# Kernel optimization log

Measured on AMD Instinct MI355X. Metric: run time of the kernel, lower is better.

## Reference

```python
import jax, jax.numpy as jnp
import numpy as np

N_NODES, N_GRAPHS, NODES_PER = 20000, 20, 1000
N_EDGES, N_REL, N_BASES = 320000, 8, 4
FEAT, HID, EMB = 128, 256, 128


def rgcn_conv(x, src, dst, etype, comp, basis, root_w, bias, num_rel, num_nodes):
    # W_r = sum_b comp[r,b] * basis[b]  (basis decomposition)
    W = jnp.einsum('rb,bio->rio', comp, basis)           # [R, in, out]
    xr = jnp.einsum('ni,rio->nro', x, W)                 # [N, R, out]
    msg = xr[src, etype]                                 # [E, out] gather per edge
    # mean aggregation per (dst, relation), as in PyG RGCNConv (aggr='mean')
    key = dst * num_rel + etype
    cnt = jax.ops.segment_sum(jnp.ones(src.shape[0], x.dtype), key,
                              num_segments=num_nodes * num_rel)
    norm = 1.0 / jnp.maximum(cnt, 1.0)
    agg = jax.ops.segment_sum(msg * norm[key][:, None], dst, num_segments=num_nodes)
    return agg + x @ root_w + bias


def setup_inputs() -> dict:
    key = jax.random.key(0)
    ks = jax.random.split(key, 16)
    x = jax.random.normal(ks[0], (N_GRAPHS, HID), jnp.float32)
    edge_attr = jax.random.uniform(ks[1], (N_EDGES, 2), jnp.float32)
    node_x = jax.random.normal(ks[2], (N_NODES, FEAT), jnp.float32)
    edge_index = jax.random.randint(ks[3], (2, N_EDGES), 0, N_NODES)
    edge_type = jax.random.randint(ks[4], (N_EDGES,), 0, N_REL)
    batch = jnp.repeat(jnp.arange(N_GRAPHS), NODES_PER)   # equal-size graphs
    nest_id = jax.random.randint(ks[5], (N_GRAPHS,), 0, N_NODES)
    s1 = 1.0 / np.sqrt(FEAT)
    s2 = 1.0 / np.sqrt(HID)
    comp1 = jax.random.normal(ks[6], (N_REL, N_BASES), jnp.float32) * 0.5
    basis1 = jax.random.normal(ks[7], (N_BASES, FEAT, HID), jnp.float32) * s1
    root1 = jax.random.normal(ks[8], (FEAT, HID), jnp.float32) * s1
    bias1 = jnp.zeros((HID,), jnp.float32)
    comp2 = jax.random.normal(ks[9], (N_REL, N_BASES), jnp.float32) * 0.5
    basis2 = jax.random.normal(ks[10], (N_BASES, HID, EMB), jnp.float32) * s2
    root2 = jax.random.normal(ks[11], (HID, EMB), jnp.float32) * s2
    bias2 = jnp.zeros((EMB,), jnp.float32)
    msg_w = jax.random.normal(ks[12], (HID, EMB), jnp.float32) * s2
    msg_b = jnp.zeros((EMB,), jnp.float32)
    return dict(x=x, edge_attr=edge_attr, node_x=node_x, edge_index=edge_index,
                edge_type=edge_type, batch=batch, nest_id=nest_id,
                comp1=comp1, basis1=basis1, root1=root1, bias1=bias1,
                comp2=comp2, basis2=basis2, root2=root2, bias2=bias2,
                msg_w=msg_w, msg_b=msg_b)


def reference(x, edge_attr, node_x, edge_index, edge_type, batch, nest_id,
              comp1, basis1, root1, bias1, comp2, basis2, root2, bias2,
              msg_w, msg_b):
    N = node_x.shape[0]
    R = comp1.shape[0]
    B = nest_id.shape[0]
    src, dst = edge_index[0], edge_index[1]
    # distance binning (computed in original forward but unused downstream)
    distances = edge_attr[:, 0]
    min_d, max_d = distances.min(), distances.max()
    bin_size = (max_d - min_d) / 3
    _binned = jnp.clip(jnp.floor((distances - min_d) / bin_size), 0, 2)
    # 2-layer RGCN encoder (keep_dims=() -> strip_node_types is identity)
    h = jax.nn.relu(rgcn_conv(node_x, src, dst, edge_type,
                              comp1, basis1, root1, bias1, R, N))
    node_emb = rgcn_conv(h, src, dst, edge_type,
                         comp2, basis2, root2, bias2, R, N)
    nest_emb = node_emb[nest_id]                 # [B, emb]
    rel_node = node_emb - nest_emb[batch]        # [N, emb]
    message_emb = x @ msg_w + msg_b              # [B, emb]
    scores = jnp.sum(rel_node * message_emb[batch], axis=-1)  # [N]
    logits = scores.reshape(B, N // B)
    return jax.nn.log_softmax(logits, axis=-1)
```

## Files before the change

### kernel.cpp

```cpp
#include <hip/hip_runtime.h>
#include <hip/hip_bf16.h>

#define NEDGE 320000
#define NNODE 20000
#define MP    20096
#define NRELS 8
#define FEAT  128
#define HID   256
#define EMB   128
#define NGRAPH 20
#define NPG   1000
#define NBASE 4
#define PAD   96

typedef __attribute__((ext_vector_type(4))) float f32x4;
typedef __attribute__((ext_vector_type(8))) __bf16 bf16x8;
typedef __attribute__((ext_vector_type(8))) unsigned short u16x8;

static __device__ __forceinline__ float bf2f(unsigned short u){
  union { unsigned int i; float f; } v; v.i = ((unsigned int)u) << 16; return v.f;
}
static __device__ __forceinline__ unsigned short f2bf(float f){
  union { float f; unsigned int i; } v; v.f = f;
  unsigned int x = v.i;
  return (unsigned short)((x + 0x7fffu + ((x >> 16) & 1u)) >> 16);
}

__device__ __forceinline__ void load_lds16(const void* g, void* l){
  __builtin_amdgcn_global_load_lds((const __attribute__((address_space(1))) void*)g,
                                   (__attribute__((address_space(3))) void*)l, 16, 0, 0);
}

__global__ void k_zeroMe(int* __restrict__ cursor,
                         const float* __restrict__ x, const float* __restrict__ mw,
                         const float* __restrict__ mb, float* __restrict__ me){
  int blk = blockIdx.x;
  if (blk < 79){
    int i = blk*256 + threadIdx.x;
    if (i < NNODE) cursor[i] = 0;
  } else {
    int id = (blk-79)*256 + threadIdx.x;
    if (id >= NGRAPH*EMB) return;
    int g = id >> 7, e = id & 127;
    float s = mb[e];
    for (int i=0;i<HID;i++) s += x[g*HID + i] * mw[i*EMB + e];
    me[id] = s;
  }
}

__global__ void k_prepScatter(const int* __restrict__ ei, const int* __restrict__ et,
                              int* __restrict__ cursor, unsigned int* __restrict__ spk,
                              const float* __restrict__ xin, unsigned short* __restrict__ xb,
                              const float* __restrict__ basis, const float* __restrict__ root,
                              unsigned short* __restrict__ Bt,
                              const float* __restrict__ basis2, const float* __restrict__ root2,
                              const float* __restrict__ me, float* __restrict__ v){
  int blk = blockIdx.x;
  if (blk < 1250){
    int e = blk*256 + threadIdx.x;
    if (e < NEDGE){
      int src = ei[e];
      int r = et[e];
      int dst = ei[NEDGE + e];
      int pos = atomicAdd(&cursor[dst], 1);
      if (pos < PAD) spk[(size_t)dst*PAD + pos] = (unsigned int)src | ((unsigned int)r << 15);
    }
  } else if (blk < 11250){
    int i = (blk-1250)*256 + threadIdx.x;
    if (i < NNODE*FEAT) xb[i] = f2bf(xin[i]);
  } else if (blk < 11890){
    int idx = (blk-11250)*256 + threadIdx.x;
    if (idx >= 256*640) return;
    int o = idx / 640, k = idx % 640;
    float val = (k < 512) ? basis[(size_t)k*256 + o] : root[(size_t)(k-512)*256 + o];
    Bt[(size_t)o*640 + k] = f2bf(val);
  } else {
    int w = threadIdx.x >> 6, lane = threadIdx.x & 63;
    int id = (blk-11890)*4 + w;
    if (id >= NGRAPH*1280) return;
    int g = id / 1280, k = id % 1280;
    const float* row = (k < 1024) ? (basis2 + (size_t)k*EMB) : (root2 + (size_t)(k-1024)*EMB);
    float2 a = *(const float2*)(row + lane*2);
    float2 m = *(const float2*)(me + g*EMB + lane*2);
    float p = a.x*m.x + a.y*m.y;
    #pragma unroll
    for (int d=32; d; d>>=1) p += __shfl_down(p, d);
    if (lane == 0) v[(size_t)g*1280 + k] = p;
  }
}

__global__ void k_agg1(const unsigned short* __restrict__ xb, const int* __restrict__ cursor,
                       const unsigned int* __restrict__ spk,
                       const float* __restrict__ comp1, unsigned short* __restrict__ s1,
                       const float* __restrict__ v, unsigned short* __restrict__ BtV){
  if (blockIdx.x >= 1250){
    int idx = (blockIdx.x-1250)*256 + threadIdx.x;
    if (idx >= 128*256) return;
    int c = idx >> 8, k = idx & 255;
    float val = 0.f;
    if (c < 80)        val = v[(size_t)(c>>2)*1280 + (c&3)*256 + k];
    else if (c < 100)  val = v[(size_t)(c-80)*1280 + 1024 + k];
    BtV[idx] = f2bf(val);
    return;
  }
  __shared__ float c1s[32];
  __shared__ float wcomb[16*32];
  if (threadIdx.x < 32) c1s[threadIdx.x] = comp1[threadIdx.x];
  __syncthreads();
  int grp = threadIdx.x >> 4, sl = threadIdx.x & 15;
  int n = blockIdx.x*16 + grp;
  int C = cursor[n]; if (C > PAD) C = PAD;
  const unsigned int* pp = spk + (size_t)n*PAD;
  if (sl < 8){
    int c = 0;
    for (int j=0;j<C;j++) c += (int)(((pp[j] >> 15) & 7) == (unsigned)sl);
    float inv = (c > 0) ? __builtin_amdgcn_rcpf((float)c) : 0.f;
    #pragma unroll
    for (int b=0;b<NBASE;b++) wcomb[grp*32 + sl*4 + b] = c1s[sl*4+b]*inv;
  }
  const float* wg = wcomb + grp*32;
  float u[NBASE][8] = {};
  int j = 0;
  for (; j+8 <= C; j += 8){
    unsigned int pk[8];
    u16x8 vv[8];
    #pragma unroll
    for (int t=0;t<8;t++) pk[t] = pp[j+t];
    #pragma unroll
    for (int t=0;t<8;t++) vv[t] = *(const u16x8*)(xb + (size_t)(pk[t] & 0x7FFF)*FEAT + sl*8);
    #pragma unroll
    for (int t=0;t<8;t++){
      const float* cr = wg + ((pk[t] >> 15) & 7)*4;
      #pragma unroll
      for (int b=0;b<NBASE;b++){
        float wb = cr[b];
        #pragma unroll
        for (int k=0;k<8;k++) u[b][k] += wb*bf2f(vv[t][k]);
      }
    }
  }
  for (; j < C; ++j){
    unsigned int pk = pp[j];
    u16x8 vv = *(const u16x8*)(xb + (size_t)(pk & 0x7FFF)*FEAT + sl*8);
    const float* cr = wg + ((pk >> 15) & 7)*4;
    #pragma unroll
    for (int b=0;b<NBASE;b++){
      float wb = cr[b];
      #pragma unroll
      for (int k=0;k<8;k++) u[b][k] += wb*bf2f(vv[k]);
    }
  }
  #pragma unroll
  for (int b=0;b<NBASE;b++){
    u16x8 o8;
    #pragma unroll
    for (int k=0;k<8;k++) o8[k] = f2bf(u[b][k]);
    *(u16x8*)(s1 + (size_t)n*(NBASE*FEAT) + b*FEAT + sl*8) = o8;
  }
}

__global__ __launch_bounds__(256, 4)
void k_gemmHD(const unsigned short* __restrict__ A0,
              const unsigned short* __restrict__ A1,
              const unsigned short* __restrict__ B1t,
              const unsigned short* __restrict__ BtV,
              const float* __restrict__ bias1,
              float* __restrict__ D)
{
  __shared__ __align__(16) unsigned short As[32*64];
  __shared__ __align__(16) unsigned short Bs[128*64];
  __shared__ __align__(16) unsigned short hs[32*256];

  const int tid = threadIdx.x;
  const int w = tid >> 6, lane = tid & 63;
  const int wr = w >> 1, wc = w & 1;
  const int m0 = blockIdx.x * 32;

  for (int half=0; half<2; ++half){
    f32x4 acc[4];
    #pragma unroll
    for (int i=0;i<4;i++) acc[i] = (f32x4){0.f,0.f,0.f,0.f};
    for (int kt=0; kt<10; ++kt){
      const int kb = kt*64;
      {
        const unsigned short* Ab; int ld, kk0;
        if (kb < 512){ Ab = A0; ld = 512; kk0 = kb; } else { Ab = A1; ld = 128; kk0 = kb-512; }
        int row = tid >> 3, slot = tid & 7;
        int srcs = slot ^ (row & 7);
        load_lds16(Ab + (size_t)(m0+row)*ld + kk0 + srcs*8, (char*)As + (w*64)*16);
      }
      #pragma unroll
      for (int t=0;t<4;t++){
        int c = t*256 + tid, row = c >> 3, slot = c & 7;
        int srcs = slot ^ (row & 7);
        load_lds16(B1t + (size_t)(half*128+row)*640 + kb + srcs*8, (char*)Bs + (t*256 + w*64)*16);
      }
      asm volatile("s_waitcnt vmcnt(0)" ::: "memory");
      __syncthreads();
      #pragma unroll
      for (int kk=0;kk<2;++kk){
        int arow = wr*16 + (lane & 15);
        int aslot = (kk*4 + (lane >> 4)) ^ (arow & 7);
        bf16x8 afr = *(const bf16x8*)(As + arow*64 + aslot*8);
        #pragma unroll
        for (int fn=0;fn<4;++fn){
          int brow = wc*64 + fn*16 + (lane & 15);
          int bslot = (kk*4 + (lane >> 4)) ^ (brow & 7);
          bf16x8 bfr = *(const bf16x8*)(Bs + brow*64 + bslot*8);
          acc[fn] = __builtin_amdgcn_mfma_f32_16x16x32_bf16(afr, bfr, acc[fn], 0, 0, 0);
        }
      }
      __syncthreads();
    }
    #pragma unroll
    for (int fn=0;fn<4;++fn){
      int col = half*128 + wc*64 + fn*16 + (lane & 15);
      float b = bias1[col];
      int s = col >> 3;
      #pragma unroll
      for (int q=0;q<4;q++){
        int row = wr*16 + (lane >> 4)*4 + q;
        float val = acc[fn][q] + b;
        val = val > 0.f ? val : 0.f;
        int p = (s & ~7) | ((s & 7) ^ (row & 7));
        hs[row*256 + p*8 + (col & 7)] = f2bf(val);
      }
    }
  }
  __syncthreads();

  f32x4 acc2[4];
  #pragma unroll
  for (int i=0;i<4;i++) acc2[i] = (f32x4){0.f,0.f,0.f,0.f};
  for (int kt=0; kt<4; ++kt){
    const int kb = kt*64;
    #pragma unroll
    for (int t=0;t<4;t++){
      int c = t*256 + tid, row = c >> 3, slot = c & 7;
      int srcs = slot ^ (row & 7);
      load_lds16(BtV + (size_t)row*256 + kb + srcs*8, (char*)Bs + (t*256 + w*64)*16);
    }
    asm volatile("s_waitcnt vmcnt(0)" ::: "memory");
    __syncthreads();
    #pragma unroll
    for (int kk=0;kk<2;++kk){
      int arow = wr*16 + (lane & 15);
      int slog = kt*8 + kk*4 + (lane >> 4);
      int ap = (slog & ~7) | ((slog & 7) ^ (arow & 7));
      bf16x8 afr = *(const bf16x8*)(hs + arow*256 + ap*8);
      #pragma unroll
      for (int fn=0;fn<4;++fn){
        int brow = wc*64 + fn*16 + (lane & 15);
        int bslot = (kk*4 + (lane >> 4)) ^ (brow & 7);
        bf16x8 bfr = *(const bf16x8*)(Bs + brow*64 + bslot*8);
        acc2[fn] = __builtin_amdgcn_mfma_f32_16x16x32_bf16(afr, bfr, acc2[fn], 0, 0, 0);
      }
    }
    __syncthreads();
  }
  #pragma unroll
  for (int fn=0;fn<4;++fn){
    int col = wc*64 + fn*16 + (lane & 15);
    #pragma unroll
    for (int q=0;q<4;q++){
      int row = m0 + wr*16 + (lane >> 4)*4 + q;
      D[(size_t)row*128 + col] = acc2[fn][q];
    }
  }
}

__global__ void k_score2(const float* __restrict__ D, const int* __restrict__ cursor,
                         const unsigned int* __restrict__ spk,
                         const float* __restrict__ comp2, const int* __restrict__ batch,
                         float* __restrict__ sc){
  __shared__ float4 c2s[8];
  __shared__ float4 wc4[16*8];
  if (threadIdx.x < 8) c2s[threadIdx.x] = ((const float4*)comp2)[threadIdx.x];
  __syncthreads();
  int grp = threadIdx.x >> 4, sl = threadIdx.x & 15;
  int n = blockIdx.x*16 + grp;
  if (n >= NNODE) return;
  int g = batch[n];
  int C = cursor[n]; if (C > PAD) C = PAD;
  const unsigned int* pp = spk + (size_t)n*PAD;
  if (sl < 8){
    int c = 0;
    for (int j=0;j<C;j++) c += (int)(((pp[j] >> 15) & 7) == (unsigned)sl);
    float inv = (c > 0) ? __builtin_amdgcn_rcpf((float)c) : 0.f;
    float4 cw = c2s[sl];
    cw.x *= inv; cw.y *= inv; cw.z *= inv; cw.w *= inv;
    wc4[grp*8 + sl] = cw;
  }
  float acc = 0.f;
  for (int j = sl; j < C; j += 16){
    unsigned int pk = pp[j];
    int s = pk & 0x7FFF;
    float4 dv = *(const float4*)(D + (size_t)s*128 + g*4);
    float4 cw = wc4[grp*8 + ((pk >> 15) & 7)];
    acc += cw.x*dv.x + cw.y*dv.y + cw.z*dv.z + cw.w*dv.w;
  }
  #pragma unroll
  for (int d=8; d; d>>=1) acc += __shfl_down(acc, d, 16);
  if (sl == 0) sc[n] = acc + D[(size_t)n*128 + 80 + g];
}

__global__ void k_lsm(const float* __restrict__ sc, float* __restrict__ out){
  __shared__ float sb[1024];
  __shared__ float red[256];
  int g = blockIdx.x, t = threadIdx.x;
  float lm = -1e30f;
  for (int j=t; j<1024; j+=256){
    float v = (j < NPG) ? sc[g*NPG + j] : -1e30f;
    sb[j] = v; lm = fmaxf(lm, v);
  }
  red[t] = lm; __syncthreads();
  for (int off=128; off; off>>=1){ if (t < off) red[t] = fmaxf(red[t], red[t+off]); __syncthreads(); }
  float mx = red[0]; __syncthreads();
  float ls = 0.f;
  for (int j=t; j<1024; j+=256){ if (j < NPG) ls += expf(sb[j] - mx); }
  red[t] = ls; __syncthreads();
  for (int off=128; off; off>>=1){ if (t < off) red[t] += red[t+off]; __syncthreads(); }
  float lse = mx + logf(red[0]);
  for (int j=t; j<NPG; j+=256) out[g*NPG + j] = sb[j] - lse;
}

extern "C" void kernel_launch(void* const* d_in, const int* in_sizes, int n_in,
                              void* d_out, int out_size, void* d_ws, size_t ws_size,
                              hipStream_t stream) {
  const float* x       = (const float*)d_in[0];
  const float* node_x  = (const float*)d_in[2];
  const int*   ei      = (const int*)d_in[3];
  const int*   et      = (const int*)d_in[4];
  const int*   batch   = (const int*)d_in[5];
  const float* comp1   = (const float*)d_in[7];
  const float* basis1  = (const float*)d_in[8];
  const float* root1   = (const float*)d_in[9];
  const float* bias1   = (const float*)d_in[10];
  const float* comp2   = (const float*)d_in[11];
  const float* basis2  = (const float*)d_in[12];
  const float* root2   = (const float*)d_in[13];
  const float* msg_w   = (const float*)d_in[15];
  const float* msg_b   = (const float*)d_in[16];
  float* out = (float*)d_out;

  char* p = (char*)d_ws;
  size_t off = 0;
  auto alloc = [&](size_t bytes) -> char* {
    char* r = p + off;
    off += (bytes + 255) & ~(size_t)255;
    return r;
  };
  int*            cursor = (int*)alloc(NNODE*4);
  unsigned int*   spk    = (unsigned int*)alloc((size_t)NNODE*PAD*4);
  unsigned short* B1t    = (unsigned short*)alloc((size_t)256*640*2);
  unsigned short* BtV    = (unsigned short*)alloc((size_t)128*256*2);
  float*          me     = (float*)alloc(NGRAPH*EMB*4);
  float*          v      = (float*)alloc((size_t)NGRAPH*1280*4);
  unsigned short* xb     = (unsigned short*)alloc((size_t)MP*FEAT*2);
  unsigned short* s1     = (unsigned short*)alloc((size_t)MP*512*2);
  float*          D      = (float*)alloc((size_t)MP*128*4);
  float*          sc     = (float*)alloc(NNODE*4);

  k_zeroMe     <<<89, 256, 0, stream>>>(cursor, x, msg_w, msg_b, me);
  k_prepScatter<<<18290, 256, 0, stream>>>(ei, et, cursor, spk, node_x, xb,
                                           basis1, root1, B1t, basis2, root2, me, v);
  k_agg1  <<<1378, 256, 0, stream>>>(xb, cursor, spk, comp1, s1, v, BtV);
  k_gemmHD<<<628, 256, 0, stream>>>(s1, xb, B1t, BtV, bias1, D);
  k_score2<<<1250, 256, 0, stream>>>(D, cursor, spk, comp2, batch, sc);
  k_lsm   <<<NGRAPH, 256, 0, stream>>>(sc, out);
}
```

Before: 101.4 us.

## Vectorize bf16 conversion and assign one wavefront per node in aggregation

The fp32-to-bf16 conversion of node features now processes four elements per thread with float4 loads and ushort4 stores, so it needs fewer blocks. The layer-1 aggregation kernel now gives each node a full 64-lane wavefront, each lane handling two features, instead of a 16-thread group with eight features per lane. This gives more parallelism, fewer registers per lane and fully coalesced 256-byte row gathers. In exchange, the per-edge index loads and the relation-count loop are repeated per wavefront, there are four times as many blocks, and each gather is narrower (4 bytes per lane).

```diff
diff --git a/kernel.cpp b/kernel.cpp
--- a/kernel.cpp
+++ b/kernel.cpp
@@ -19,6 +19,12 @@
 
 static __device__ __forceinline__ float bf2f(unsigned short u){
   union { unsigned int i; float f; } v; v.i = ((unsigned int)u) << 16; return v.f;
+}
+static __device__ __forceinline__ float bflo(unsigned int u){
+  union { unsigned int i; float f; } v; v.i = u << 16; return v.f;
+}
+static __device__ __forceinline__ float bfhi(unsigned int u){
+  union { unsigned int i; float f; } v; v.i = u & 0xFFFF0000u; return v.f;
 }
 static __device__ __forceinline__ unsigned short f2bf(float f){
   union { float f; unsigned int i; } v; v.f = f;
@@ -65,18 +71,23 @@
       int pos = atomicAdd(&cursor[dst], 1);
       if (pos < PAD) spk[(size_t)dst*PAD + pos] = (unsigned int)src | ((unsigned int)r << 15);
     }
-  } else if (blk < 11250){
-    int i = (blk-1250)*256 + threadIdx.x;
-    if (i < NNODE*FEAT) xb[i] = f2bf(xin[i]);
-  } else if (blk < 11890){
-    int idx = (blk-11250)*256 + threadIdx.x;
+  } else if (blk < 3750){
+    int i = (blk-1250)*1024 + threadIdx.x*4;
+    if (i < NNODE*FEAT){
+      float4 f = *(const float4*)(xin + i);
+      ushort4 o;
+      o.x = f2bf(f.x); o.y = f2bf(f.y); o.z = f2bf(f.z); o.w = f2bf(f.w);
+      *(ushort4*)(xb + i) = o;
+    }
+  } else if (blk < 4390){
+    int idx = (blk-3750)*256 + threadIdx.x;
     if (idx >= 256*640) return;
     int o = idx / 640, k = idx % 640;
     float val = (k < 512) ? basis[(size_t)k*256 + o] : root[(size_t)(k-512)*256 + o];
     Bt[(size_t)o*640 + k] = f2bf(val);
   } else {
     int w = threadIdx.x >> 6, lane = threadIdx.x & 63;
-    int id = (blk-11890)*4 + w;
+    int id = (blk-4390)*4 + w;
     if (id >= NGRAPH*1280) return;
     int g = id / 1280, k = id % 1280;
     const float* row = (k < 1024) ? (basis2 + (size_t)k*EMB) : (root2 + (size_t)(k-1024)*EMB);
@@ -93,8 +104,8 @@
                        const unsigned int* __restrict__ spk,
                        const float* __restrict__ comp1, unsigned short* __restrict__ s1,
                        const float* __restrict__ v, unsigned short* __restrict__ BtV){
-  if (blockIdx.x >= 1250){
-    int idx = (blockIdx.x-1250)*256 + threadIdx.x;
+  if (blockIdx.x >= 5000){
+    int idx = (blockIdx.x-5000)*256 + threadIdx.x;
     if (idx >= 128*256) return;
     int c = idx >> 8, k = idx & 255;
     float val = 0.f;
@@ -104,58 +115,51 @@
     return;
   }
   __shared__ float c1s[32];
-  __shared__ float wcomb[16*32];
+  __shared__ float wcomb[4][32];
   if (threadIdx.x < 32) c1s[threadIdx.x] = comp1[threadIdx.x];
   __syncthreads();
-  int grp = threadIdx.x >> 4, sl = threadIdx.x & 15;
-  int n = blockIdx.x*16 + grp;
+  int w = threadIdx.x >> 6, lane = threadIdx.x & 63;
+  int n = blockIdx.x*4 + w;
   int C = cursor[n]; if (C > PAD) C = PAD;
   const unsigned int* pp = spk + (size_t)n*PAD;
-  if (sl < 8){
+  if (lane < 8){
     int c = 0;
-    for (int j=0;j<C;j++) c += (int)(((pp[j] >> 15) & 7) == (unsigned)sl);
+    for (int j=0;j<C;j++) c += (int)(((pp[j] >> 15) & 7) == (unsigned)lane);
     float inv = (c > 0) ? __builtin_amdgcn_rcpf((float)c) : 0.f;
     #pragma unroll
-    for (int b=0;b<NBASE;b++) wcomb[grp*32 + sl*4 + b] = c1s[sl*4+b]*inv;
-  }
-  const float* wg = wcomb + grp*32;
-  float u[NBASE][8] = {};
+    for (int b=0;b<NBASE;b++) wcomb[w][lane*4+b] = c1s[lane*4+b]*inv;
+  }
+  const float* wg = wcomb[w];
+  float u0[NBASE] = {0,0,0,0}, u1[NBASE] = {0,0,0,0};
+  const unsigned int* xrow;
   int j = 0;
   for (; j+8 <= C; j += 8){
-    unsigned int pk[8];
-    u16x8 vv[8];
+    unsigned int pk[8], vv[8];
     #pragma unroll
     for (int t=0;t<8;t++) pk[t] = pp[j+t];
     #pragma unroll
-    for (int t=0;t<8;t++) vv[t] = *(const u16x8*)(xb + (size_t)(pk[t] & 0x7FFF)*FEAT + sl*8);
+    for (int t=0;t<8;t++)
+      vv[t] = *(const unsigned int*)(xb + (size_t)(pk[t] & 0x7FFF)*FEAT + lane*2);
     #pragma unroll
     for (int t=0;t<8;t++){
       const float* cr = wg + ((pk[t] >> 15) & 7)*4;
-      #pragma unroll
-      for (int b=0;b<NBASE;b++){
-        float wb = cr[b];
-        #pragma unroll
-        for (int k=0;k<8;k++) u[b][k] += wb*bf2f(vv[t][k]);
-      }
+      float a = bflo(vv[t]), b = bfhi(vv[t]);
+      #pragma unroll
+      for (int q=0;q<NBASE;q++){ u0[q] += cr[q]*a; u1[q] += cr[q]*b; }
     }
   }
   for (; j < C; ++j){
     unsigned int pk = pp[j];
-    u16x8 vv = *(const u16x8*)(xb + (size_t)(pk & 0x7FFF)*FEAT + sl*8);
+    unsigned int vv = *(const unsigned int*)(xb + (size_t)(pk & 0x7FFF)*FEAT + lane*2);
     const float* cr = wg + ((pk >> 15) & 7)*4;
-    #pragma unroll
-    for (int b=0;b<NBASE;b++){
-      float wb = cr[b];
-      #pragma unroll
-      for (int k=0;k<8;k++) u[b][k] += wb*bf2f(vv[k]);
-    }
+    float a = bflo(vv), b = bfhi(vv);
+    #pragma unroll
+    for (int q=0;q<NBASE;q++){ u0[q] += cr[q]*a; u1[q] += cr[q]*b; }
   }
   #pragma unroll
   for (int b=0;b<NBASE;b++){
-    u16x8 o8;
-    #pragma unroll
-    for (int k=0;k<8;k++) o8[k] = f2bf(u[b][k]);
-    *(u16x8*)(s1 + (size_t)n*(NBASE*FEAT) + b*FEAT + sl*8) = o8;
+    unsigned int pack = (unsigned int)f2bf(u0[b]) | ((unsigned int)f2bf(u1[b]) << 16);
+    *(unsigned int*)(s1 + (size_t)n*512 + b*FEAT + lane*2) = pack;
   }
 }
 
@@ -362,9 +366,9 @@
   float*          sc     = (float*)alloc(NNODE*4);
 
   k_zeroMe     <<<89, 256, 0, stream>>>(cursor, x, msg_w, msg_b, me);
-  k_prepScatter<<<18290, 256, 0, stream>>>(ei, et, cursor, spk, node_x, xb,
+  k_prepScatter<<<10790, 256, 0, stream>>>(ei, et, cursor, spk, node_x, xb,
                                            basis1, root1, B1t, basis2, root2, me, v);
-  k_agg1  <<<1378, 256, 0, stream>>>(xb, cursor, spk, comp1, s1, v, BtV);
+  k_agg1  <<<5128, 256, 0, stream>>>(xb, cursor, spk, comp1, s1, v, BtV);
   k_gemmHD<<<628, 256, 0, stream>>>(s1, xb, B1t, BtV, bias1, D);
   k_score2<<<1250, 256, 0, stream>>>(D, cursor, spk, comp2, batch, sc);
   k_lsm   <<<NGRAPH, 256, 0, stream>>>(sc, out);
```

Result: slower. 107.7 us (+6.1%).
